# Kernel tuning notes

Measured on AMD Instinct MI355X. Metric: run time of the kernel, lower is better.

Reference implementation:

```python
import jax, jax.numpy as jnp
import numpy as np

IN_CH = 512
SCALES = (128.0, 256.0, 512.0)
ASPECT_RATIOS = (0.5, 1.0, 2.0)
NUM_ANCHORS = 9
PRE_NMS_TOPK = 10000
POST_NMS_TOPK = 2000
NMS_THRESH = 0.7


def conv2d(x, w, b, pad):
    y = jax.lax.conv_general_dilated(
        x, w, window_strides=(1, 1), padding=[(pad, pad), (pad, pad)],
        dimension_numbers=('NCHW', 'OIHW', 'NCHW'))
    return y + b[None, :, None, None]


def generate_anchors(image_hw, feat_hw, dtype=jnp.float32):
    img_h, img_w = image_hw
    gh, gw = feat_hw
    stride_h = img_h // gh
    stride_w = img_w // gw
    scale = jnp.asarray(SCALES, dtype)
    ar = jnp.asarray(ASPECT_RATIOS, dtype)
    h_ratio = jnp.sqrt(ar)
    w_ratio = 1.0 / h_ratio
    ws = (w_ratio[:, None] * scale[None, :]).reshape(-1)  # (9,) ratio-major
    hs = (h_ratio[:, None] * scale[None, :]).reshape(-1)
    base = jnp.round(jnp.stack([-ws, -hs, ws, hs], axis=1) / 2.0)  # (9,4)
    shift_x = jnp.arange(gw, dtype=dtype) * stride_w
    shift_y = jnp.arange(gh, dtype=dtype) * stride_h
    sy, sx = jnp.meshgrid(shift_y, shift_x, indexing='ij')
    sx = sx.reshape(-1)
    sy = sy.reshape(-1)
    shifts = jnp.stack([sx, sy, sx, sy], axis=1)  # (gh*gw, 4)
    anchors = (shifts[:, None, :] + base[None, :, :]).reshape(-1, 4)
    return anchors


def decode_boxes(deltas, anchors):
    # deltas: (N,4) [dx,dy,dw,dh]; anchors: (N,4) [x1,y1,x2,y2]
    w = anchors[:, 2] - anchors[:, 0]
    h = anchors[:, 3] - anchors[:, 1]
    cx = anchors[:, 0] + 0.5 * w
    cy = anchors[:, 1] + 0.5 * h
    dx, dy, dw, dh = deltas[:, 0], deltas[:, 1], deltas[:, 2], deltas[:, 3]
    pcx = w * dx + cx
    pcy = h * dy + cy
    pw = jnp.exp(dw) * w
    ph = jnp.exp(dh) * h
    return jnp.stack([pcx - 0.5 * pw, pcy - 0.5 * ph,
                      pcx + 0.5 * pw, pcy + 0.5 * ph], axis=1)


def clamp_boxes(b, image_hw):
    h, w = image_hw
    return jnp.stack([jnp.clip(b[:, 0], 0.0, w), jnp.clip(b[:, 1], 0.0, h),
                      jnp.clip(b[:, 2], 0.0, w), jnp.clip(b[:, 3], 0.0, h)], axis=1)


def pairwise_iou(boxes1, boxes2):
    area1 = (boxes1[:, 2] - boxes1[:, 0]) * (boxes1[:, 3] - boxes1[:, 1])
    area2 = (boxes2[:, 2] - boxes2[:, 0]) * (boxes2[:, 3] - boxes2[:, 1])
    xl = jnp.maximum(boxes1[:, None, 0], boxes2[None, :, 0])
    yt = jnp.maximum(boxes1[:, None, 1], boxes2[None, :, 1])
    xr = jnp.minimum(boxes1[:, None, 2], boxes2[None, :, 2])
    yb = jnp.minimum(boxes1[:, None, 3], boxes2[None, :, 3])
    inter = jnp.clip(xr - xl, 0.0) * jnp.clip(yb - yt, 0.0)
    return inter / (area1[:, None] + area2[None, :] - inter)


def nms_keep(boxes_sorted, thresh):
    # boxes already sorted by score descending; returns bool keep mask
    n = boxes_sorted.shape[0]
    iou = pairwise_iou(boxes_sorted, boxes_sorted)  # (n,n) ~ the memory-bound hot spot
    idx = jnp.arange(n)
    def body(i, keep):
        suppressed = jnp.any((iou[i] > thresh) & keep & (idx < i))
        return keep.at[i].set(jnp.logical_not(suppressed))
    return jax.lax.fori_loop(0, n, body, jnp.ones((n,), dtype=bool))


def filter_proposals(proposals, logits, image_hw):
    scores = jax.nn.sigmoid(logits.reshape(-1))
    top_scores, top_idx = jax.lax.top_k(scores, PRE_NMS_TOPK)  # sorted descending
    props = proposals[top_idx]
    props = clamp_boxes(props, image_hw)
    keep = nms_keep(jax.lax.stop_gradient(props), NMS_THRESH)
    masked = jnp.where(keep, jax.lax.stop_gradient(top_scores), -1.0)
    sel_scores, sel = jax.lax.top_k(masked, POST_NMS_TOPK)
    valid = sel_scores >= 0.0  # sigmoid scores are >0; padded slots are -1
    out_boxes = jnp.where(valid[:, None], props[sel], 0.0)
    out_scores = jnp.where(valid, top_scores[sel], 0.0)
    return out_boxes, out_scores


def setup_inputs() -> dict:
    key = jax.random.key(0)
    ks = jax.random.split(key, 6)
    image = jax.random.normal(ks[0], (1, 3, 800, 800), jnp.float32)
    feat = jax.random.normal(ks[1], (1, IN_CH, 50, 50), jnp.float32)
    # small init scales keep exp(dw) numerically tame (mimics real conv init)
    rpn_w = jax.random.normal(ks[2], (IN_CH, IN_CH, 3, 3), jnp.float32) * 0.02
    rpn_b = jnp.zeros((IN_CH,), jnp.float32)
    cls_w = jax.random.normal(ks[3], (NUM_ANCHORS, IN_CH, 1, 1), jnp.float32) * 0.01
    cls_b = jnp.zeros((NUM_ANCHORS,), jnp.float32)
    box_w = jax.random.normal(ks[4], (NUM_ANCHORS * 4, IN_CH, 1, 1), jnp.float32) * 0.01
    box_b = jnp.zeros((NUM_ANCHORS * 4,), jnp.float32)
    return {"image": image, "feat": feat, "rpn_w": rpn_w, "rpn_b": rpn_b,
            "cls_w": cls_w, "cls_b": cls_b, "box_w": box_w, "box_b": box_b}


def reference(image, feat, rpn_w, rpn_b, cls_w, cls_b, box_w, box_b):
    B, _, H, W = feat.shape  # B == 1 as in the original (single-image RPN)
    rpn_feat = jax.nn.relu(conv2d(feat, rpn_w, rpn_b, pad=1))
    cls = conv2d(rpn_feat, cls_w, cls_b, pad=0)        # (1, 9, H, W)
    box = conv2d(rpn_feat, box_w, box_b, pad=0)        # (1, 36, H, W)
    anchors = generate_anchors(image.shape[-2:], (H, W), feat.dtype)  # (H*W*9, 4)
    # cls: NCHW -> NHWC -> (N_anchors, 1), anchor order = (y, x, anchor)
    cls_flat = jnp.transpose(cls, (0, 2, 3, 1)).reshape(-1, 1)
    # box: (1,9,4,H,W) -> (1,H,W,9,4) -> (N_anchors, 4)
    deltas = jnp.transpose(box.reshape(B, NUM_ANCHORS, 4, H, W), (0, 3, 4, 1, 2)).reshape(-1, 4)
    proposals = decode_boxes(deltas, anchors)
    props, scores = filter_proposals(proposals, jax.lax.stop_gradient(cls_flat), image.shape[-2:])
    return props, scores, cls_flat
```

## Files before the change

### kernel.cpp

```cpp
#include <hip/hip_runtime.h>
#include <cstdint>
#include <cstddef>


typedef unsigned long long ull;
typedef double d4 __attribute__((ext_vector_type(4)));

#define NANCH 9
#define NPIX  2500
#define CIN   512
#define COUT  512
#define KTOT  4608
#define KSEG  2304
#define NBOX  22500
#define TOPK1 10000
#define TOPK2 2000
#define WORDS 157
#define NHEAD 45
#define HPAD  48

__global__ __launch_bounds__(256) void wtrans(const float* __restrict__ w,
                                              float* __restrict__ wT) {
  __shared__ float t[36][65];
  const int ci0 = blockIdx.x * 4;
  const int co0 = blockIdx.y * 64;
  const int tid = threadIdx.x;
  const int co_l = tid >> 2, cq = tid & 3;
  const float* src = w + (size_t)(co0 + co_l) * KTOT + (ci0 + cq) * 9;
#pragma unroll
  for (int r = 0; r < 9; ++r) t[r * 4 + cq][co_l] = src[r];
  __syncthreads();
  const int co_w = tid & 63, rw0 = tid >> 6;
#pragma unroll
  for (int m = 0; m < 9; ++m) {
    int rw = rw0 + 4 * m;
    int tap = rw >> 2, cqq = rw & 3;
    wT[((size_t)tap * 512 + ci0 + cqq) * 512 + co0 + co_w] = t[rw][co_w];
  }
}

__global__ __launch_bounds__(256, 5) void conv_gemm(const float* __restrict__ feat,
                                                    const float* __restrict__ wT,
                                                    double* __restrict__ part) {
  const int p0  = blockIdx.x * 32;
  const int co0 = blockIdx.y * 64;
  const int z   = blockIdx.z;
  const int kseg0 = z * KSEG;
  __shared__ float As[2][32][40];
  __shared__ float Bs[2][32][72];
  const int tid  = threadIdx.x;
  const int lane = tid & 63;
  const int wave = tid >> 6;
  const int quad = lane >> 4;
  const int l16  = lane & 15;
  const int wp = (wave & 1) * 16;
  const int wc = (wave >> 1) * 32;
  const int plA = tid & 31, kAr = tid >> 5;
  const int pB = p0 + plA;
  const int py = pB / 50, px = pB - py * 50;
  const int coB = tid & 63, kBr = tid >> 6;

  int pmap[4];
  {
    double av_p = (quad == 0) ? (double)(l16 + 1) : (quad == 1 ? 1.0 : 0.0);
    double bv_p = (quad == 0) ? 1.0 : (quad == 1 ? (double)(1000 * (l16 + 1)) : 0.0);
    d4 dp = (d4){0.0, 0.0, 0.0, 0.0};
    dp = __builtin_amdgcn_mfma_f64_16x16x4f64(av_p, bv_p, dp, 0, 0, 0);
#pragma unroll
    for (int r = 0; r < 4; ++r) {
      int iv = (int)(dp[r] + 0.5);
      int mm = iv % 1000 - 1;
      int nn = iv / 1000 - 1;
      pmap[r] = (mm & 255) | (nn << 8);
    }
  }

  d4 acc[2];
#pragma unroll
  for (int i = 0; i < 2; ++i) acc[i] = (d4){0.0, 0.0, 0.0, 0.0};

  const int NCH = KSEG / 32;

  float fa[4], fb[8];

  auto loadA = [&](int cc) {
    int kk0 = kseg0 + cc * 32;
    int tap = kk0 >> 9;
    int ci0 = kk0 & 511;
    int ky = (tap * 11) >> 5;
    int kx = tap - 3 * ky;
    int yy = py + ky - 1, xx = px + kx - 1;
    bool valid = (pB < NPIX) && (yy >= 0) && (yy < 50) && (xx >= 0) && (xx < 50);
    int off = valid ? ((ci0 + kAr) * NPIX + yy * 50 + xx) : 0;
#pragma unroll
    for (int jj = 0; jj < 4; ++jj) {
      float v = feat[off + jj * 8 * NPIX];
      fa[jj] = valid ? v : 0.0f;
    }
  };
  auto loadB = [&](int cc) {
    const float* src = wT + (size_t)(kseg0 + cc * 32 + kBr) * 512 + co0 + coB;
#pragma unroll
    for (int s = 0; s < 8; ++s) fb[s] = src[s * 4 * 512];
  };

  loadA(0);
  loadB(0);
#pragma unroll
  for (int jj = 0; jj < 4; ++jj) As[0][kAr + 8 * jj][plA] = fa[jj];
#pragma unroll
  for (int s = 0; s < 8; ++s) Bs[0][kBr + 4 * s][coB] = fb[s];
  loadA(1);
  loadB(1);
  __syncthreads();

  for (int c = 0; c < NCH; ++c) {
    const int buf = c & 1;
    if (c + 1 < NCH) {
#pragma unroll
      for (int jj = 0; jj < 4; ++jj) As[buf ^ 1][kAr + 8 * jj][plA] = fa[jj];
#pragma unroll
      for (int s = 0; s < 8; ++s) Bs[buf ^ 1][kBr + 4 * s][coB] = fb[s];
    }
    if (c + 2 < NCH) {
      loadA(c + 2);
      loadB(c + 2);
    }
#pragma unroll
    for (int kk = 0; kk < 32; kk += 4) {
      double av  = (double)As[buf][kk + quad][wp + l16];
      double bv0 = (double)Bs[buf][kk + quad][wc + l16];
      double bv1 = (double)Bs[buf][kk + quad][wc + 16 + l16];
      acc[0] = __builtin_amdgcn_mfma_f64_16x16x4f64(av, bv0, acc[0], 0, 0, 0);
      acc[1] = __builtin_amdgcn_mfma_f64_16x16x4f64(av, bv1, acc[1], 0, 0, 0);
    }
    __syncthreads();
  }
  double* basez = part + (size_t)z * COUT * NPIX;
#pragma unroll
  for (int cj = 0; cj < 2; ++cj) {
#pragma unroll
    for (int r = 0; r < 4; ++r) {
      int mm = pmap[r] & 255, nn = pmap[r] >> 8;
      int p  = p0 + wp + mm;
      int co = co0 + wc + cj * 16 + nn;
      if (p < NPIX) basez[(size_t)co * NPIX + p] = acc[cj][r];
    }
  }
}

__global__ __launch_bounds__(256) void heads_mm(
    const double* __restrict__ part, const float* __restrict__ rpn_b,
    const float* __restrict__ cls_w, const float* __restrict__ box_w,
    double* __restrict__ headsc) {
  const int lane = threadIdx.x & 63;
  const int o = __builtin_amdgcn_readfirstlane(blockIdx.y * 4 + (threadIdx.x >> 6));
  if (o >= NHEAD) return;
  const int p = blockIdx.x * 64 + lane;
  const bool act = p < NPIX;
  const int pp = act ? p : 0;
  const float* wsel = (o < 9) ? (cls_w + (size_t)o * CIN)
                              : (box_w + (size_t)(o - 9) * CIN);
  const double* p0 = part + pp;
  const double* p1 = part + (size_t)COUT * NPIX + pp;
  double acc = 0.0;
#pragma unroll 4
  for (int co = 0; co < CIN; ++co) {
    double v = p0[(size_t)co * NPIX] + p1[(size_t)co * NPIX] + (double)rpn_b[co];
    v = v > 0.0 ? v : 0.0;
    acc += (double)wsel[co] * v;
  }
  if (act) headsc[(size_t)p * HPAD + o] = acc;
}

__global__ __launch_bounds__(256) void decode_kernel(
    const double* __restrict__ headsc, const float* __restrict__ cls_b,
    const float* __restrict__ box_b, double* __restrict__ logits,
    double* __restrict__ boxesAll, float* __restrict__ out_cls) {
  int idx = blockIdx.x * blockDim.x + threadIdx.x;
  if (idx >= NBOX) return;
  int p = idx / 9, a = idx - p * 9;
  int y = p / 50, x = p - y * 50;
  double sx = 16.0 * (double)x, sy = 16.0 * (double)y;
  const double scs[3] = {128.0, 256.0, 512.0};
  const double ars[3] = {0.5, 1.0, 2.0};
  double ar = ars[a / 3], sc = scs[a - (a / 3) * 3];
  double hr = sqrt(ar), wr = 1.0 / hr;
  double wv = wr * sc, hv = hr * sc;
  double bx0 = rint(-wv * 0.5), by0 = rint(-hv * 0.5);
  double bx1 = rint(wv * 0.5), by1 = rint(hv * 0.5);
  double a0 = sx + bx0, a1 = sy + by0, a2 = sx + bx1, a3 = sy + by1;
  double wA = a2 - a0, hA = a3 - a1;
  double cx = a0 + 0.5 * wA, cy = a1 + 0.5 * hA;
  const double* hp = headsc + (size_t)p * HPAD;
  double dx = hp[9 + a * 4 + 0] + (double)box_b[a * 4 + 0];
  double dy = hp[9 + a * 4 + 1] + (double)box_b[a * 4 + 1];
  double dw = hp[9 + a * 4 + 2] + (double)box_b[a * 4 + 2];
  double dh = hp[9 + a * 4 + 3] + (double)box_b[a * 4 + 3];
  double pcx = wA * dx + cx, pcy = hA * dy + cy;
  double pw = exp(dw) * wA, ph = exp(dh) * hA;
  double b0 = pcx - 0.5 * pw, b1 = pcy - 0.5 * ph;
  double b2 = pcx + 0.5 * pw, b3 = pcy + 0.5 * ph;
  b0 = fmin(fmax(b0, 0.0), 800.0);
  b1 = fmin(fmax(b1, 0.0), 800.0);
  b2 = fmin(fmax(b2, 0.0), 800.0);
  b3 = fmin(fmax(b3, 0.0), 800.0);
  boxesAll[(size_t)idx * 4 + 0] = b0;
  boxesAll[(size_t)idx * 4 + 1] = b1;
  boxesAll[(size_t)idx * 4 + 2] = b2;
  boxesAll[(size_t)idx * 4 + 3] = b3;
  double L = hp[a] + (double)cls_b[a];
  logits[idx] = L;
  out_cls[idx] = (float)L;
}

__global__ __launch_bounds__(256) void rank_count(const double* __restrict__ logits,
                                                  int* __restrict__ ranks) {
  __shared__ double Ls[2048];
  int i = blockIdx.x * 256 + threadIdx.x;
  int j0 = blockIdx.y * 2048;
  int jn = NBOX - j0;
  if (jn > 2048) jn = 2048;
  for (int t = threadIdx.x; t < jn; t += 256) Ls[t] = logits[j0 + t];
  __syncthreads();
  if (i >= NBOX) return;
  double Li = logits[i];
  int cnt = 0;
  for (int t = 0; t < jn; ++t) {
    double Lj = Ls[t];
    int j = j0 + t;
    cnt += (Lj > Li || (Lj == Li && j < i)) ? 1 : 0;
  }
  atomicAdd(&ranks[i], cnt);
}

__global__ __launch_bounds__(256) void scatter_topk(const double* __restrict__ logits,
                                                    const double* __restrict__ boxesAll,
                                                    const int* __restrict__ ranks,
                                                    double* __restrict__ sLog,
                                                    double* __restrict__ sBox) {
  int i = blockIdx.x * 256 + threadIdx.x;
  if (i >= NBOX) return;
  int r = ranks[i];
  if (r < TOPK1) {
    sLog[r] = logits[i];
    sBox[(size_t)r * 4 + 0] = boxesAll[(size_t)i * 4 + 0];
    sBox[(size_t)r * 4 + 1] = boxesAll[(size_t)i * 4 + 1];
    sBox[(size_t)r * 4 + 2] = boxesAll[(size_t)i * 4 + 2];
    sBox[(size_t)r * 4 + 3] = boxesAll[(size_t)i * 4 + 3];
  }
}

__global__ __launch_bounds__(256) void iou_mask(const double* __restrict__ sb,
                                                ull* __restrict__ mask) {
  const int it = blockIdx.x;
  const int wt = blockIdx.y;
  if (wt * 4 + 3 < it) return;
  __shared__ double ib[64][4];
  __shared__ double jb[256][4];
  const int tid = threadIdx.x;
  {
    int ii = it * 64 + (tid >> 2);
    int d = tid & 3;
    ib[tid >> 2][d] = (ii < TOPK1) ? sb[(size_t)ii * 4 + d] : 0.0;
  }
  for (int t = tid; t < 1024; t += 256) {
    int jj = wt * 256 + (t >> 2);
    jb[t >> 2][t & 3] = (jj < TOPK1) ? sb[(size_t)jj * 4 + (t & 3)] : 0.0;
  }
  __syncthreads();
  const int il = tid & 63, wl = tid >> 6;
  const int i = it * 64 + il;
  const int word = wt * 4 + wl;
  if (i >= TOPK1 || word >= WORDS || word < (i >> 6)) return;
  const double x0 = ib[il][0], y0 = ib[il][1], x1 = ib[il][2], y1 = ib[il][3];
  const double areai = (x1 - x0) * (y1 - y0);
  ull bits = 0;
  const int jbase = word * 64;
  for (int b = 0; b < 64; ++b) {
    int j = jbase + b;
    if (j <= i || j >= TOPK1) continue;
    int jl = wl * 64 + b;
    double u0 = jb[jl][0], u1 = jb[jl][1], u2 = jb[jl][2], u3 = jb[jl][3];
    double xl = fmax(x0, u0), yt = fmax(y0, u1);
    double xr = fmin(x1, u2), yb = fmin(y1, u3);
    double iw = xr - xl, ih = yb - yt;
    iw = iw > 0.0 ? iw : 0.0;
    ih = ih > 0.0 ? ih : 0.0;
    double inter = iw * ih;
    double aj = (u2 - u0) * (u3 - u1);
    double un = areai + aj - inter;
    if (inter > 0.7 * un) bits |= 1ull << b;
  }
  mask[(size_t)word * TOPK1 + i] = bits;
}

#define NTILE 8
#define TRS   9
#define KCAP  2112

__global__ __launch_bounds__(256) void nms_scan(const ull* __restrict__ mask,
                                                ull* __restrict__ keepwords) {
  __shared__ ull tileRows[512 * TRS];
  __shared__ int klist[KCAP];
  __shared__ ull remvPart[32][NTILE + 1];
  __shared__ unsigned int remv32[NTILE * 2];
  __shared__ int newk[64];
  __shared__ int kcLds, nkLds, doneLds;
  const int tid = threadIdx.x;
  const int lane = tid & 63;
  const int wave = tid >> 6;
  if (tid == 0) { kcLds = 0; nkLds = 0; doneLds = 0; }
  __syncthreads();

  for (int T = 0; T < (WORDS + NTILE - 1) / NTILE; ++T) {
    const int G0 = T * NTILE;
    const int TW = (WORDS - G0 < NTILE) ? (WORDS - G0) : NTILE;
    const int kc0 = kcLds;
#pragma unroll
    for (int pass = 0; pass < 8; ++pass) {
      int lr = pass * 64 + lane;
      int w0 = wave * 2;
      int gr = G0 * 64 + lr;
      ull v0 = 0, v1 = 0;
      if (gr < TOPK1) {
        if (w0 < TW)     v0 = mask[(size_t)(G0 + w0) * TOPK1 + gr];
        if (w0 + 1 < TW) v1 = mask[(size_t)(G0 + w0 + 1) * TOPK1 + gr];
      }
      tileRows[lr * TRS + w0]     = v0;
      tileRows[lr * TRS + w0 + 1] = v1;
    }
    {
      int w = tid & 7, stripe = tid >> 3;
      ull acc = 0;
      if (w < TW) {
        const ull* mw = mask + (size_t)(G0 + w) * TOPK1;
        int t = stripe;
        for (; t + 224 < kc0; t += 256) {
          ull a0 = mw[klist[t      ]];
          ull a1 = mw[klist[t +  32]];
          ull a2 = mw[klist[t +  64]];
          ull a3 = mw[klist[t +  96]];
          ull a4 = mw[klist[t + 128]];
          ull a5 = mw[klist[t + 160]];
          ull a6 = mw[klist[t + 192]];
          ull a7 = mw[klist[t + 224]];
          acc |= ((a0 | a1) | (a2 | a3)) | ((a4 | a5) | (a6 | a7));
        }
        for (; t < kc0; t += 32) acc |= mw[klist[t]];
      }
      remvPart[stripe][w] = acc;
    }
    __syncthreads();
    if (tid < NTILE) {
      ull r = 0;
#pragma unroll
      for (int s = 0; s < 32; ++s) r |= remvPart[s][tid];
      remv32[tid * 2]     = (unsigned int)r;
      remv32[tid * 2 + 1] = (unsigned int)(r >> 32);
    }
    __syncthreads();
    for (int gi = 0; gi < TW; ++gi) {
      const int g = G0 + gi;
      if (wave == 0) {
        ull cur = ((ull)remv32[gi * 2 + 1] << 32) | remv32[gi * 2];
        unsigned int clo = __builtin_amdgcn_readfirstlane((unsigned int)cur);
        unsigned int chi = __builtin_amdgcn_readfirstlane((unsigned int)(cur >> 32));
        cur = ((ull)chi << 32) | clo;
        ull mrow = tileRows[(gi * 64 + lane) * TRS + gi];
        const unsigned int ml = (unsigned int)mrow;
        const unsigned int mh = (unsigned int)(mrow >> 32);
        const ull validm = (g == WORDS - 1) ? 0xFFFFull : ~0ull;
        ull rem = (~cur) & validm;
        while (rem) {
          int b = __ffsll((long long)rem) - 1;
          b = __builtin_amdgcn_readfirstlane(b);
          ull m = ((ull)(unsigned int)__builtin_amdgcn_readlane((int)mh, b) << 32) |
                  (unsigned int)__builtin_amdgcn_readlane((int)ml, b);
          cur |= m;
          ull above = (b == 63) ? 0ull : (~0ull << (b + 1));
          rem = (~cur) & rem & above;
        }
        ull kb = (~cur) & validm;
        if (lane == 0) keepwords[g] = kb;
        int kc = kcLds;
        if ((kb >> lane) & 1ull) {
          int ofs = __popcll(lane ? (kb & ((1ull << lane) - 1ull)) : 0ull);
          klist[kc + ofs] = g * 64 + lane;
          newk[ofs] = gi * 64 + lane;
        }
        if (lane == 0) {
          int nk = __popcll(kb);
          nkLds = nk;
          kcLds = kc + nk;
          doneLds = (kc + nk >= TOPK2) ? 1 : 0;
        }
      }
      __syncthreads();
      if (doneLds) break;
      if (gi + 1 < TW) {
        int w = tid & 7, k0 = tid >> 3;
        int nk = nkLds;
        if (w > gi && w < TW) {
          ull acc = 0;
          for (int kk = k0; kk < nk; kk += 32) acc |= tileRows[newk[kk] * TRS + w];
          if (acc) {
            atomicOr(&remv32[w * 2], (unsigned int)acc);
            atomicOr(&remv32[w * 2 + 1], (unsigned int)(acc >> 32));
          }
        }
      }
      __syncthreads();
    }
    if (doneLds) break;
  }
}

__global__ __launch_bounds__(256) void finalize_kernel(const ull* __restrict__ keepwords,
                                                       const double* __restrict__ sBox,
                                                       const double* __restrict__ sLog,
                                                       float* __restrict__ out) {
  __shared__ int pref[WORDS];
  int t = threadIdx.x;
  if (t == 0) {
    int s = 0;
    for (int w = 0; w < WORDS; ++w) {
      pref[w] = s;
      s += __popcll(keepwords[w]);
    }
  }
  __syncthreads();
  if (t < WORDS) {
    ull kb = keepwords[t];
    int base = pref[t];
    while (kb) {
      int b = __ffsll((long long)kb) - 1;
      kb &= kb - 1;
      if (base < TOPK2) {
        int i = t * 64 + b;
        out[base * 4 + 0] = (float)sBox[(size_t)i * 4 + 0];
        out[base * 4 + 1] = (float)sBox[(size_t)i * 4 + 1];
        out[base * 4 + 2] = (float)sBox[(size_t)i * 4 + 2];
        out[base * 4 + 3] = (float)sBox[(size_t)i * 4 + 3];
        double L = sLog[i];
        out[TOPK2 * 4 + base] = (float)(1.0 / (1.0 + exp(-L)));
      }
      ++base;
    }
  }
}

extern "C" void kernel_launch(void* const* d_in, const int* in_sizes, int n_in,
                              void* d_out, int out_size, void* d_ws, size_t ws_size,
                              hipStream_t stream) {
  const float* feat  = (const float*)d_in[1];
  const float* rpn_w = (const float*)d_in[2];
  const float* rpn_b = (const float*)d_in[3];
  const float* cls_w = (const float*)d_in[4];
  const float* cls_b = (const float*)d_in[5];
  const float* box_w = (const float*)d_in[6];
  const float* box_b = (const float*)d_in[7];
  float* out = (float*)d_out;

  char* ws = (char*)d_ws;
  double* part     = (double*)(ws);
  double* logits   = (double*)(ws + 20480000);
  double* boxesAll = (double*)(ws + 20660000);
  int*    ranks    = (int*)   (ws + 21380000);
  double* sBox     = (double*)(ws + 21470000);
  double* sLog     = (double*)(ws + 21790000);
  ull*    mask     = (ull*)   (ws + 21870000);
  ull*    keepw    = (ull*)   (ws + 34430000);
  float*  wT       = (float*) (ws + 21870000);
  double* headsc   = (double*)(ws + 21870000);

  hipMemsetAsync(d_out, 0, (TOPK2 * 4 + TOPK2) * sizeof(float), stream);
  hipMemsetAsync(ranks, 0, NBOX * sizeof(int), stream);
  hipMemsetAsync(keepw, 0, WORDS * sizeof(ull), stream);

  wtrans<<<dim3(128, 8), 256, 0, stream>>>(rpn_w, wT);
  conv_gemm<<<dim3(80, 8, 2), 256, 0, stream>>>(feat, wT, part);
  heads_mm<<<dim3(40, 12), 256, 0, stream>>>(part, rpn_b, cls_w, box_w, headsc);
  decode_kernel<<<88, 256, 0, stream>>>(headsc, cls_b, box_b, logits, boxesAll,
                                        out + TOPK2 * 5);
  rank_count<<<dim3(88, 11), 256, 0, stream>>>(logits, ranks);
  scatter_topk<<<88, 256, 0, stream>>>(logits, boxesAll, ranks, sLog, sBox);
  iou_mask<<<dim3(WORDS, 40), 256, 0, stream>>>(sBox, mask);
  nms_scan<<<1, 256, 0, stream>>>(mask, keepw);
  finalize_kernel<<<1, 256, 0, stream>>>(keepw, sBox, sLog, out);
}
```

Before: 820.9 us.

## Pipeline NMS scan tiles: prefetch next tile while wave 0 resolves current

Restructures the sequential NMS scan so wave 0 processes the whole tile of 8 words alone, using shuffles instead of block-wide barriers and atomics per word. Meanwhile the other three waves load the next tile's mask rows into a second LDS buffer and OR in suppression from previously kept boxes. A short catch-up pass then adds suppression from boxes kept in the current tile. The aim is to remove per-word __syncthreads and to hide global mask latency behind the serial scan. The cost is double the LDS for tile rows and a serial bottleneck on one wave.

```diff
diff --git a/kernel.cpp b/kernel.cpp
--- a/kernel.cpp
+++ b/kernel.cpp
@@ -298,76 +298,51 @@
 #define NTILE 8
 #define TRS   9
 #define KCAP  2112
+#define NT    ((WORDS + NTILE - 1) / NTILE)
 
 __global__ __launch_bounds__(256) void nms_scan(const ull* __restrict__ mask,
                                                 ull* __restrict__ keepwords) {
-  __shared__ ull tileRows[512 * TRS];
+  __shared__ ull tileRows[2][512 * TRS];
   __shared__ int klist[KCAP];
   __shared__ ull remvPart[32][NTILE + 1];
-  __shared__ unsigned int remv32[NTILE * 2];
+  __shared__ ull remvA[NTILE];
   __shared__ int newk[64];
-  __shared__ int kcLds, nkLds, doneLds;
+  __shared__ int kcLds, doneLds;
   const int tid = threadIdx.x;
   const int lane = tid & 63;
   const int wave = tid >> 6;
-  if (tid == 0) { kcLds = 0; nkLds = 0; doneLds = 0; }
-  __syncthreads();
-
-  for (int T = 0; T < (WORDS + NTILE - 1) / NTILE; ++T) {
+
+  if (tid == 0) { kcLds = 0; doneLds = 0; }
+  if (tid < NTILE) remvA[tid] = 0;
+  __syncthreads();
+
+  for (int idx = tid; idx < NTILE * 512; idx += 256) {
+    int w = idx >> 9, row = idx & 511;
+    ull v = (row < TOPK1) ? mask[(size_t)w * TOPK1 + row] : 0;
+    tileRows[0][row * TRS + w] = v;
+  }
+  __syncthreads();
+
+  int buf = 0;
+  for (int T = 0; T < NT; ++T) {
     const int G0 = T * NTILE;
     const int TW = (WORDS - G0 < NTILE) ? (WORDS - G0) : NTILE;
-    const int kc0 = kcLds;
-#pragma unroll
-    for (int pass = 0; pass < 8; ++pass) {
-      int lr = pass * 64 + lane;
-      int w0 = wave * 2;
-      int gr = G0 * 64 + lr;
-      ull v0 = 0, v1 = 0;
-      if (gr < TOPK1) {
-        if (w0 < TW)     v0 = mask[(size_t)(G0 + w0) * TOPK1 + gr];
-        if (w0 + 1 < TW) v1 = mask[(size_t)(G0 + w0 + 1) * TOPK1 + gr];
-      }
-      tileRows[lr * TRS + w0]     = v0;
-      tileRows[lr * TRS + w0 + 1] = v1;
-    }
-    {
-      int w = tid & 7, stripe = tid >> 3;
-      ull acc = 0;
-      if (w < TW) {
-        const ull* mw = mask + (size_t)(G0 + w) * TOPK1;
-        int t = stripe;
-        for (; t + 224 < kc0; t += 256) {
-          ull a0 = mw[klist[t      ]];
-          ull a1 = mw[klist[t +  32]];
-          ull a2 = mw[klist[t +  64]];
-          ull a3 = mw[klist[t +  96]];
-          ull a4 = mw[klist[t + 128]];
-          ull a5 = mw[klist[t + 160]];
-          ull a6 = mw[klist[t + 192]];
-          ull a7 = mw[klist[t + 224]];
-          acc |= ((a0 | a1) | (a2 | a3)) | ((a4 | a5) | (a6 | a7));
+    const int kcStart = kcLds;
+    const int G0n = G0 + NTILE;
+    const int TWn = (WORDS - G0n < NTILE) ? (WORDS - G0n) : NTILE;
+
+    if (wave == 0) {
+      int kc = kcStart;
+      int done = 0;
+      for (int gi = 0; gi < TW; ++gi) {
+        const int g = G0 + gi;
+        ull cur = remvA[gi];
+        {
+          unsigned int clo = __builtin_amdgcn_readfirstlane((unsigned int)cur);
+          unsigned int chi = __builtin_amdgcn_readfirstlane((unsigned int)(cur >> 32));
+          cur = ((ull)chi << 32) | clo;
         }
-        for (; t < kc0; t += 32) acc |= mw[klist[t]];
-      }
-      remvPart[stripe][w] = acc;
-    }
-    __syncthreads();
-    if (tid < NTILE) {
-      ull r = 0;
-#pragma unroll
-      for (int s = 0; s < 32; ++s) r |= remvPart[s][tid];
-      remv32[tid * 2]     = (unsigned int)r;
-      remv32[tid * 2 + 1] = (unsigned int)(r >> 32);
-    }
-    __syncthreads();
-    for (int gi = 0; gi < TW; ++gi) {
-      const int g = G0 + gi;
-      if (wave == 0) {
-        ull cur = ((ull)remv32[gi * 2 + 1] << 32) | remv32[gi * 2];
-        unsigned int clo = __builtin_amdgcn_readfirstlane((unsigned int)cur);
-        unsigned int chi = __builtin_amdgcn_readfirstlane((unsigned int)(cur >> 32));
-        cur = ((ull)chi << 32) | clo;
-        ull mrow = tileRows[(gi * 64 + lane) * TRS + gi];
+        ull mrow = tileRows[buf][(gi * 64 + lane) * TRS + gi];
         const unsigned int ml = (unsigned int)mrow;
         const unsigned int mh = (unsigned int)(mrow >> 32);
         const ull validm = (g == WORDS - 1) ? 0xFFFFull : ~0ull;
@@ -383,36 +358,80 @@
         }
         ull kb = (~cur) & validm;
         if (lane == 0) keepwords[g] = kb;
-        int kc = kcLds;
+        int nk = __popcll(kb);
         if ((kb >> lane) & 1ull) {
           int ofs = __popcll(lane ? (kb & ((1ull << lane) - 1ull)) : 0ull);
           klist[kc + ofs] = g * 64 + lane;
           newk[ofs] = gi * 64 + lane;
         }
-        if (lane == 0) {
-          int nk = __popcll(kb);
-          nkLds = nk;
-          kcLds = kc + nk;
-          doneLds = (kc + nk >= TOPK2) ? 1 : 0;
+        kc += nk;
+        if (kc >= TOPK2) done = 1;
+        if (!done && gi + 1 < TW && nk > 0) {
+          int w = lane & 7, s = lane >> 3;
+          ull d = 0;
+          for (int kk = s; kk < nk; kk += 8)
+            d |= tileRows[buf][newk[kk] * TRS + w];
+          d |= __shfl_xor(d, 8);
+          d |= __shfl_xor(d, 16);
+          d |= __shfl_xor(d, 32);
+          if (s == 0 && w > gi && w < TW) remvA[w] |= d;
         }
+        if (done) break;
       }
-      __syncthreads();
-      if (doneLds) break;
-      if (gi + 1 < TW) {
-        int w = tid & 7, k0 = tid >> 3;
-        int nk = nkLds;
-        if (w > gi && w < TW) {
-          ull acc = 0;
-          for (int kk = k0; kk < nk; kk += 32) acc |= tileRows[newk[kk] * TRS + w];
-          if (acc) {
-            atomicOr(&remv32[w * 2], (unsigned int)acc);
-            atomicOr(&remv32[w * 2 + 1], (unsigned int)(acc >> 32));
-          }
+      if (lane == 0) {
+        kcLds = kc;
+        if (kc >= TOPK2) doneLds = 1;
+      }
+    } else if (T + 1 < NT) {
+      const int tid3 = tid - 64;
+      for (int idx = tid3; idx < TWn * 512; idx += 192) {
+        int w = idx >> 9, row = idx & 511;
+        int gr = G0n * 64 + row;
+        ull v = (gr < TOPK1) ? mask[(size_t)(G0n + w) * TOPK1 + gr] : 0;
+        tileRows[buf ^ 1][row * TRS + w] = v;
+      }
+      int w = tid3 & 7, stripe = tid3 >> 3;
+      ull acc = 0;
+      if (w < TWn) {
+        const ull* mw = mask + (size_t)(G0n + w) * TOPK1;
+        int t = stripe;
+        for (; t + 7 * 24 < kcStart; t += 8 * 24) {
+          ull a0 = mw[klist[t          ]];
+          ull a1 = mw[klist[t + 1 * 24]];
+          ull a2 = mw[klist[t + 2 * 24]];
+          ull a3 = mw[klist[t + 3 * 24]];
+          ull a4 = mw[klist[t + 4 * 24]];
+          ull a5 = mw[klist[t + 5 * 24]];
+          ull a6 = mw[klist[t + 6 * 24]];
+          ull a7 = mw[klist[t + 7 * 24]];
+          acc |= ((a0 | a1) | (a2 | a3)) | ((a4 | a5) | (a6 | a7));
         }
+        for (; t < kcStart; t += 24) acc |= mw[klist[t]];
       }
-      __syncthreads();
-    }
+      remvPart[stripe][w] = acc;
+    }
+    __syncthreads();
     if (doneLds) break;
+    if (T + 1 >= NT) break;
+    const int kcNew = kcLds;
+    if (wave == 0) {
+      int w = lane & 7, s = lane >> 3;
+      ull d = 0;
+      if (w < TWn) {
+        const ull* mw = mask + (size_t)(G0n + w) * TOPK1;
+        for (int kk = kcStart + s; kk < kcNew; kk += 8) d |= mw[klist[kk]];
+      }
+      remvPart[24 + s][w] = d;
+    }
+    __syncthreads();
+    if (tid < NTILE) {
+      ull r = 0;
+#pragma unroll
+      for (int s2 = 0; s2 < 32; ++s2) r |= remvPart[s2][tid];
+      remvA[tid] = r;
+    }
+    __syncthreads();
+    buf ^= 1;
   }
 }
 
```

Result: slower. 852.8 us (+3.9%).
